# Optimization experiments

Hardware: AMD Instinct MI355X
Metric: run time of the kernel (lower is better)

The kernel has to match this reference:

```python
import jax, jax.numpy as jnp
import numpy as np

L, D, H, DK, FF, R, N, B = 8, 256, 8, 32, 1024, 37, 1024, 1
EPS = 1e-6


def setup_inputs() -> dict:
    key = jax.random.key(0)
    ks = jax.random.split(key, 16)
    def w(i, shape, s=0.05):
        return jax.random.normal(ks[i], shape, jnp.float32) * s
    return {
        "x": jax.random.normal(ks[0], (B, N, D), jnp.float32),
        "relations": jax.random.randint(ks[1], (N, N), 0, R),
        "Wq": w(2, (L, D, D)), "bq": jnp.zeros((L, D), jnp.float32),
        "Wk": w(3, (L, D, D)), "bk": jnp.zeros((L, D), jnp.float32),
        "Wv": w(4, (L, D, D)), "bv": jnp.zeros((L, D), jnp.float32),
        "Wo": w(5, (L, D, D)), "bo": jnp.zeros((L, D), jnp.float32),
        "rel_k_emb": w(6, (L, R, DK)), "rel_v_emb": w(7, (L, R, DK)),
        "W1": w(8, (L, D, FF)), "b1": jnp.zeros((L, FF), jnp.float32),
        "W2": w(9, (L, FF, D)), "b2": jnp.zeros((L, D), jnp.float32),
        "ln1_g": jnp.ones((L, D), jnp.float32), "ln1_b": jnp.zeros((L, D), jnp.float32),
        "ln2_g": jnp.ones((L, D), jnp.float32), "ln2_b": jnp.zeros((L, D), jnp.float32),
        "lnf_g": jnp.ones((D,), jnp.float32), "lnf_b": jnp.zeros((D,), jnp.float32),
    }


def _layernorm(h, g, b):
    # Annotated-Transformer LayerNorm: g*(x-mu)/(std+eps)+b with unbiased std
    mu = h.mean(-1, keepdims=True)
    sd = jnp.sqrt(h.var(-1, keepdims=True, ddof=1))
    return g * (h - mu) / (sd + EPS) + b


def reference(x, relations, Wq, bq, Wk, bk, Wv, bv, Wo, bo,
              rel_k_emb, rel_v_emb, W1, b1, W2, b2,
              ln1_g, ln1_b, ln2_g, ln2_b, lnf_g, lnf_b):
    Bb, n, d = x.shape
    scale = 1.0 / jnp.sqrt(jnp.float32(DK))
    for l in range(L):
        # --- relation-aware self-attention sublayer (pre-norm residual) ---
        xn = _layernorm(x, ln1_g[l], ln1_b[l])
        q = (xn @ Wq[l] + bq[l]).reshape(Bb, n, H, DK).transpose(0, 2, 1, 3)
        k = (xn @ Wk[l] + bk[l]).reshape(Bb, n, H, DK).transpose(0, 2, 1, 3)
        v = (xn @ Wv[l] + bv[l]).reshape(Bb, n, H, DK).transpose(0, 2, 1, 3)
        rk = rel_k_emb[l][relations]  # [n, n, DK] irregular gather
        rv = rel_v_emb[l][relations]  # [n, n, DK]
        scores = (jnp.einsum('bhid,bhjd->bhij', q, k)
                  + jnp.einsum('bhid,ijd->bhij', q, rk)) * scale
        p = jax.nn.softmax(scores, axis=-1)
        o = (jnp.einsum('bhij,bhjd->bhid', p, v)
             + jnp.einsum('bhij,ijd->bhid', p, rv))
        o = o.transpose(0, 2, 1, 3).reshape(Bb, n, d) @ Wo[l] + bo[l]
        x = x + o
        # --- position-wise FFN sublayer (pre-norm residual) ---
        xn = _layernorm(x, ln2_g[l], ln2_b[l])
        x = x + (jax.nn.relu(xn @ W1[l] + b1[l]) @ W2[l] + b2[l])
    return _layernorm(x, lnf_g, lnf_b)
```

## Files before the change

kernel.cpp:

```cpp
#include <hip/hip_runtime.h>
#include <stdint.h>

#define L_ 8
#define D_ 256
#define H_ 8
#define DK_ 32
#define FF_ 1024
#define R_ 37
#define N_ 1024
#define JS_ 4

#define SCL (0.17677669529663689f * 1.4426950408889634f)

typedef float f4v __attribute__((ext_vector_type(4)));
typedef short b8v __attribute__((ext_vector_type(8)));
typedef uint  u2v __attribute__((ext_vector_type(2)));

__device__ __forceinline__ ushort f2b(float f){
  union { float f; uint32_t u; } x; x.f = f;
  return (ushort)((x.u + 0x7FFFu + ((x.u >> 16) & 1u)) >> 16);
}
__device__ __forceinline__ float b2f(ushort u){
  union { uint32_t u; float f; } x; x.u = ((uint32_t)u) << 16;
  return x.f;
}
__device__ __forceinline__ uint pk2b(float lo, float hi){
  return (((uint)f2b(hi)) << 16) | (uint)f2b(lo);
}
__device__ __forceinline__ float ex2(float x){ return __builtin_amdgcn_exp2f(x); }

__global__ __launch_bounds__(256)
void wcast_kernel(const float* __restrict__ src, ushort* __restrict__ dst, int K, int Nc){
  __shared__ float t[32][33];
  int l = blockIdx.z;
  long base = (long)l * K * Nc;
  int n0 = blockIdx.x * 32, k0 = blockIdx.y * 32;
  int tx = threadIdx.x, ty = threadIdx.y;
  #pragma unroll
  for (int r = 0; r < 32; r += 8)
    t[ty + r][tx] = src[base + (long)(k0 + ty + r) * Nc + n0 + tx];
  __syncthreads();
  #pragma unroll
  for (int r = 0; r < 32; r += 8)
    dst[base + (long)(n0 + ty + r) * K + k0 + tx] = f2b(t[tx][ty + r]);
}

template<int OUTB>
__global__ __launch_bounds__(64)
void ln_kernel(const float* __restrict__ x, const float* __restrict__ g, const float* __restrict__ b,
               ushort* __restrict__ ob, float* __restrict__ of){
  int row = blockIdx.x, lane = threadIdx.x;
  float4 v = ((const float4*)(x + (long)row * D_))[lane];
  float s = v.x + v.y + v.z + v.w;
  float s2 = v.x*v.x + v.y*v.y + v.z*v.z + v.w*v.w;
  #pragma unroll
  for (int o = 32; o; o >>= 1){ s += __shfl_xor(s, o); s2 += __shfl_xor(s2, o); }
  float mu = s * (1.f / D_);
  float var = (s2 - D_ * mu * mu) * (1.f / (D_ - 1));
  var = fmaxf(var, 0.f);
  float inv = 1.f / (sqrtf(var) + 1e-6f);
  float4 gv = ((const float4*)g)[lane];
  float4 bv = ((const float4*)b)[lane];
  float o0 = gv.x * (v.x - mu) * inv + bv.x;
  float o1 = gv.y * (v.y - mu) * inv + bv.y;
  float o2 = gv.z * (v.z - mu) * inv + bv.z;
  float o3 = gv.w * (v.w - mu) * inv + bv.w;
  if (OUTB){
    ushort4 u; u.x = f2b(o0); u.y = f2b(o1); u.z = f2b(o2); u.w = f2b(o3);
    ((ushort4*)ob)[(long)row * 64 + lane] = u;
  } else {
    float4 o; o.x = o0; o.y = o1; o.z = o2; o.w = o3;
    ((float4*)of)[(long)row * 64 + lane] = o;
  }
}

template<int QKV, int RELU, int RESID, int OUTF, int OUTB>
__global__ __launch_bounds__(256)
void gemm_kernel(const ushort* __restrict__ A,
                 const ushort* __restrict__ W0, const ushort* __restrict__ W1p, const ushort* __restrict__ W2p,
                 const float* __restrict__ B0, const float* __restrict__ B1p, const float* __restrict__ B2p,
                 float* __restrict__ resid, float* __restrict__ outF, ushort* __restrict__ outB,
                 int M, int Nc, int K){
  __shared__ ushort Al[64 * 48];
  __shared__ ushort Bl[64 * 48];
  int tid = threadIdx.x;
  int lane = tid & 63, w = tid >> 6;
  int wm = w >> 1, wn = w & 1;
  int bn0 = blockIdx.x * 64, bm0 = blockIdx.y * 64;
  const ushort* WT; const float* bias; int wn0;
  if (QKV){
    int which = bn0 >> 8;
    WT = which == 0 ? W0 : (which == 1 ? W1p : W2p);
    bias = which == 0 ? B0 : (which == 1 ? B1p : B2p);
    wn0 = bn0 & 255;
  } else { WT = W0; bias = B0; wn0 = bn0; }

  int r4 = tid >> 2, c8 = (tid & 3) * 8;
  const ushort* ag = A + (long)(bm0 + r4) * K + c8;
  const ushort* bg = WT + (long)(wn0 + r4) * K + c8;

  f4v acc[2][2];
  #pragma unroll
  for (int i = 0; i < 2; ++i)
    #pragma unroll
    for (int j = 0; j < 2; ++j)
      acc[i][j] = (f4v){0.f, 0.f, 0.f, 0.f};

  int l16 = lane & 15, lg = lane >> 4;
  int arow0 = (wm * 32 + l16) * 48 + lg * 8;
  int brow0 = (wn * 32 + l16) * 48 + lg * 8;

  for (int k0 = 0; k0 < K; k0 += 32){
    b8v a8 = *(const b8v*)(ag + k0);
    b8v b8 = *(const b8v*)(bg + k0);
    __syncthreads();
    *(b8v*)&Al[r4 * 48 + c8] = a8;
    *(b8v*)&Bl[r4 * 48 + c8] = b8;
    __syncthreads();
    b8v a0 = *(const b8v*)&Al[arow0];
    b8v a1 = *(const b8v*)&Al[arow0 + 16 * 48];
    b8v b0 = *(const b8v*)&Bl[brow0];
    b8v b1 = *(const b8v*)&Bl[brow0 + 16 * 48];
    acc[0][0] = __builtin_amdgcn_mfma_f32_16x16x32_bf16(a0, b0, acc[0][0], 0, 0, 0);
    acc[0][1] = __builtin_amdgcn_mfma_f32_16x16x32_bf16(a0, b1, acc[0][1], 0, 0, 0);
    acc[1][0] = __builtin_amdgcn_mfma_f32_16x16x32_bf16(a1, b0, acc[1][0], 0, 0, 0);
    acc[1][1] = __builtin_amdgcn_mfma_f32_16x16x32_bf16(a1, b1, acc[1][1], 0, 0, 0);
  }
  #pragma unroll
  for (int fi = 0; fi < 2; ++fi)
    #pragma unroll
    for (int fj = 0; fj < 2; ++fj)
      #pragma unroll
      for (int j = 0; j < 4; ++j){
        int row = bm0 + wm * 32 + fi * 16 + lg * 4 + j;
        int col = bn0 + wn * 32 + fj * 16 + l16;
        float v = acc[fi][fj][j] + bias[QKV ? (col & 255) : col];
        if (QKV){
          long idx = (long)(col >> 8) * 262144 + (long)(((col >> 5) & 7) << 15) + (row << 5) + (col & 31);
          outB[idx] = f2b(v);
        } else {
          if (RELU) v = fmaxf(v, 0.f);
          long idx = (long)row * Nc + col;
          if (RESID) v += resid[idx];
          if (OUTF) outF[idx] = v;
          if (OUTB) outB[idx] = f2b(v);
        }
      }
}

__global__ __launch_bounds__(256)
void vt_kernel(const ushort* __restrict__ vb, ushort* __restrict__ vbt){
  __shared__ ushort t[64][36];
  int j0 = blockIdx.x * 64, h = blockIdx.y;
  int tid = threadIdx.x;
  {
    int r = tid >> 2, c = (tid & 3) * 8;
    *(b8v*)&t[r][c] = *(const b8v*)(vb + ((long)(h << 10) + j0 + r) * 32 + c);
  }
  __syncthreads();
  int d = tid >> 3, jj = (tid & 7) * 8;
  b8v o;
  #pragma unroll
  for (int e = 0; e < 8; ++e) o[e] = (short)t[jj + e][d];
  *(b8v*)(vbt + (long)(h * 32 + d) * 1024 + j0 + jj) = o;
}

__global__ __launch_bounds__(320)
void qr_kernel(const ushort* __restrict__ qb, const float* __restrict__ rke, float* __restrict__ qr){
  __shared__ float ql[256];
  int i = blockIdx.x, t = threadIdx.x;
  if (t < 256){
    int h = t >> 5, dk = t & 31;
    ql[t] = b2f(qb[(long)((h << 10) + i) * 32 + dk]);
  }
  __syncthreads();
  if (t < H_ * R_){
    int h = t / R_, r = t - h * R_;
    const float* qh = &ql[h * DK_];
    const float* e = rke + r * DK_;
    float acc = 0.f;
    #pragma unroll
    for (int d = 0; d < DK_; ++d) acc += qh[d] * e[d];
    qr[((long)(h << 10) + i) * 40 + r] = acc * SCL;
  }
}

__global__ __launch_bounds__(256)
void attn_kernel(const ushort* __restrict__ qb, const ushort* __restrict__ kb,
                 const ushort* __restrict__ vbt, const float* __restrict__ qr,
                 const int* __restrict__ rel, float* __restrict__ part){
  __shared__ ushort q_l[64 * 40];
  __shared__ ushort k_l[32 * 40];
  __shared__ ushort vt_l[32 * 40];
  __shared__ int    rel_l[64 * 36];
  __shared__ float  qr_l[64 * 40];
  __shared__ float  prb[64 * 40];
  __shared__ uint   p_l[4 * 16 * 20];

  int tid = threadIdx.x, lane = tid & 63, w = tid >> 6;
  int l16 = lane & 15, g = lane >> 4;
  int ib0 = blockIdx.x * 64, h = blockIdx.y, js = blockIdx.z;
  int i_loc = w * 16 + l16;

  {
    int r = tid >> 2, c8 = (tid & 3) * 8;
    *(b8v*)&q_l[r * 40 + c8] = *(const b8v*)(qb + (long)((h << 10) + ib0 + r) * 32 + c8);
  }
  {
    const float* src = qr + (long)((h << 10) + ib0) * 40;
    for (int idx = tid; idx < 2560; idx += 256){ qr_l[idx] = src[idx]; prb[idx] = 0.f; }
  }
  __syncthreads();

  b8v qf = *(const b8v*)&q_l[i_loc * 40 + g * 8];

  f4v oacc0 = (f4v){0.f,0.f,0.f,0.f}, oacc1 = (f4v){0.f,0.f,0.f,0.f};
  float m = -3.0e38f, lsum = 0.f;
  const float* qrr = &qr_l[i_loc * 40];

  for (int jt = 0; jt < 8; ++jt){
    int j0 = js * 256 + jt * 32;
    __syncthreads();
    if (tid < 128){
      int r = tid >> 2, c8 = (tid & 3) * 8;
      *(b8v*)&k_l[r * 40 + c8] = *(const b8v*)(kb + (long)((h << 10) + j0 + r) * 32 + c8);
    } else {
      int t2 = tid - 128;
      int d0 = t2 >> 2, c8 = (t2 & 3) * 8;
      *(b8v*)&vt_l[d0 * 40 + c8] = *(const b8v*)(vbt + (long)(h * 32 + d0) * 1024 + j0 + c8);
    }
    {
      int r = tid >> 3, c = (tid & 7) * 4;
      *(int4*)&rel_l[r * 36 + c] = *(const int4*)(rel + (long)(ib0 + r) * N_ + j0 + c);
      *(int4*)&rel_l[(r + 32) * 36 + c] = *(const int4*)(rel + (long)(ib0 + r + 32) * N_ + j0 + c);
    }
    __syncthreads();

    b8v kf0 = *(const b8v*)&k_l[l16 * 40 + g * 8];
    b8v kf1 = *(const b8v*)&k_l[(16 + l16) * 40 + g * 8];
    f4v z = (f4v){0.f,0.f,0.f,0.f};
    f4v s0 = __builtin_amdgcn_mfma_f32_16x16x32_bf16(kf0, qf, z, 0, 0, 0);
    f4v s1 = __builtin_amdgcn_mfma_f32_16x16x32_bf16(kf1, qf, z, 0, 0, 0);

    int4 r0 = *(const int4*)&rel_l[i_loc * 36 + g * 4];
    int4 r1 = *(const int4*)&rel_l[i_loc * 36 + 16 + g * 4];
    int rix[8] = { r0.x, r0.y, r0.z, r0.w, r1.x, r1.y, r1.z, r1.w };
    float sv[8];
    #pragma unroll
    for (int e = 0; e < 4; ++e){
      sv[e]     = s0[e] * SCL + qrr[rix[e]];
      sv[e + 4] = s1[e] * SCL + qrr[rix[e + 4]];
    }
    float tmax = sv[0];
    #pragma unroll
    for (int e = 1; e < 8; ++e) tmax = fmaxf(tmax, sv[e]);
    tmax = fmaxf(tmax, __shfl_xor(tmax, 16));
    tmax = fmaxf(tmax, __shfl_xor(tmax, 32));
    float mn = fmaxf(m, tmax);
    float f = ex2(m - mn);
    float p[8]; float ps = 0.f;
    #pragma unroll
    for (int e = 0; e < 8; ++e){ p[e] = ex2(sv[e] - mn); ps += p[e]; }
    ps += __shfl_xor(ps, 16);
    ps += __shfl_xor(ps, 32);
    lsum = lsum * f + ps;
    oacc0 *= f; oacc1 *= f;
    if (mn > m){
      #pragma unroll
      for (int b2 = 0; b2 < 10; ++b2){
        int bi = g * 10 + b2;
        if (bi < R_) prb[i_loc * 40 + bi] *= f;
      }
    }
    m = mn;
    #pragma unroll
    for (int e = 0; e < 8; ++e) atomicAdd(&prb[i_loc * 40 + rix[e]], p[e]);

    uint pk0 = pk2b(p[0], p[1]), pk1 = pk2b(p[2], p[3]);
    uint pk2 = pk2b(p[4], p[5]), pk3 = pk2b(p[6], p[7]);
    uint* pw = &p_l[w * 320 + l16 * 20];
    *(u2v*)&pw[g * 2]     = (u2v){pk0, pk1};
    *(u2v*)&pw[8 + g * 2] = (u2v){pk2, pk3};
    b8v pf = *(const b8v*)&pw[g * 4];
    b8v vt0 = *(const b8v*)&vt_l[l16 * 40 + g * 8];
    b8v vt1 = *(const b8v*)&vt_l[(16 + l16) * 40 + g * 8];
    oacc0 = __builtin_amdgcn_mfma_f32_16x16x32_bf16(vt0, pf, oacc0, 0, 0, 0);
    oacc1 = __builtin_amdgcn_mfma_f32_16x16x32_bf16(vt1, pf, oacc1, 0, 0, 0);
  }

  float* pp = part + ((long)(h * JS_ + js) * N_ + ib0 + i_loc) * 72;
  #pragma unroll
  for (int r2 = 0; r2 < 4; ++r2){
    pp[g * 4 + r2] = oacc0[r2];
    pp[16 + g * 4 + r2] = oacc1[r2];
  }
  #pragma unroll
  for (int b2 = 0; b2 < 10; ++b2){
    int bi = g * 10 + b2;
    if (bi < R_) pp[32 + bi] = prb[i_loc * 40 + bi];
  }
  if (g == 0){ pp[69] = m; pp[70] = lsum; }
}

__global__ __launch_bounds__(256)
void combine_kernel(const float* __restrict__ part, const float* __restrict__ rve,
                    ushort* __restrict__ ob){
  __shared__ float prl[4][40];
  int tid = threadIdx.x, lane = tid & 63, w = tid >> 6;
  int i = blockIdx.x * 4 + w, h = blockIdx.y;
  int d = lane & 31;
  const float* pb = part + ((long)h * JS_) * N_ * 72 + (long)i * 72;
  float ms[JS_], ls[JS_], wf[JS_];
  float mstar = -3.0e38f;
  #pragma unroll
  for (int s = 0; s < JS_; ++s){
    ms[s] = pb[(long)s * N_ * 72 + 69];
    ls[s] = pb[(long)s * N_ * 72 + 70];
    mstar = fmaxf(mstar, ms[s]);
  }
  float lstar = 0.f;
  #pragma unroll
  for (int s = 0; s < JS_; ++s){ wf[s] = ex2(ms[s] - mstar); lstar += ls[s] * wf[s]; }
  float o1d = 0.f;
  #pragma unroll
  for (int s = 0; s < JS_; ++s) o1d += pb[(long)s * N_ * 72 + d] * wf[s];
  if (lane < R_){
    float prv = 0.f;
    #pragma unroll
    for (int s = 0; s < JS_; ++s) prv += pb[(long)s * N_ * 72 + 32 + lane] * wf[s];
    prl[w][lane] = prv;
  }
  float o2 = 0.f;
  for (int r = 0; r < R_; ++r) o2 += prl[w][r] * rve[r * DK_ + d];
  float val = (o1d + o2) / lstar;
  if (lane < 32) ob[(long)i * D_ + h * DK_ + d] = f2b(val);
}

extern "C" void kernel_launch(void* const* d_in, const int* in_sizes, int n_in,
                              void* d_out, int out_size, void* d_ws, size_t ws_size,
                              hipStream_t stream){
  const float* x    = (const float*)d_in[0];
  const int*   rel  = (const int*)d_in[1];
  const float* Wq   = (const float*)d_in[2];
  const float* bq   = (const float*)d_in[3];
  const float* Wk   = (const float*)d_in[4];
  const float* bk   = (const float*)d_in[5];
  const float* Wv   = (const float*)d_in[6];
  const float* bv   = (const float*)d_in[7];
  const float* Wo   = (const float*)d_in[8];
  const float* bo   = (const float*)d_in[9];
  const float* rke  = (const float*)d_in[10];
  const float* rve  = (const float*)d_in[11];
  const float* W1   = (const float*)d_in[12];
  const float* b1   = (const float*)d_in[13];
  const float* W2   = (const float*)d_in[14];
  const float* b2   = (const float*)d_in[15];
  const float* ln1g = (const float*)d_in[16];
  const float* ln1b = (const float*)d_in[17];
  const float* ln2g = (const float*)d_in[18];
  const float* ln2b = (const float*)d_in[19];
  const float* lnfg = (const float*)d_in[20];
  const float* lnfb = (const float*)d_in[21];

  char* wsb = (char*)d_ws;
  size_t off = 0;
  auto alloc = [&](size_t bytes){ void* p = wsb + off; off += (bytes + 255) & ~255ull; return p; };
  float*  xw   = (float*) alloc((size_t)N_ * D_ * 4);
  ushort* qkvb = (ushort*)alloc((size_t)3 * H_ * N_ * DK_ * 2);
  ushort* vbt  = (ushort*)alloc((size_t)H_ * DK_ * N_ * 2);
  float*  qr   = (float*) alloc((size_t)H_ * N_ * 40 * 4);
  ushort* xnb  = (ushort*)alloc((size_t)N_ * D_ * 2);
  ushort* obf  = (ushort*)alloc((size_t)N_ * D_ * 2);
  float*  part = (float*) alloc((size_t)H_ * JS_ * N_ * 72 * 4);
  ushort* hidb = (ushort*)part;
  ushort* wqT  = (ushort*)alloc((size_t)L_ * D_ * D_ * 2);
  ushort* wkT  = (ushort*)alloc((size_t)L_ * D_ * D_ * 2);
  ushort* wvT  = (ushort*)alloc((size_t)L_ * D_ * D_ * 2);
  ushort* woT  = (ushort*)alloc((size_t)L_ * D_ * D_ * 2);
  ushort* w1T  = (ushort*)alloc((size_t)L_ * D_ * FF_ * 2);
  ushort* w2T  = (ushort*)alloc((size_t)L_ * D_ * FF_ * 2);
  (void)ws_size; (void)in_sizes; (void)n_in; (void)out_size;

  ushort* qb = qkvb;
  ushort* kb = qkvb + (size_t)H_ * N_ * DK_;
  ushort* vb = qkvb + (size_t)2 * H_ * N_ * DK_;

  dim3 tb(32, 8);
  wcast_kernel<<<dim3(D_/32,  D_/32,  L_), tb, 0, stream>>>(Wq, wqT, D_, D_);
  wcast_kernel<<<dim3(D_/32,  D_/32,  L_), tb, 0, stream>>>(Wk, wkT, D_, D_);
  wcast_kernel<<<dim3(D_/32,  D_/32,  L_), tb, 0, stream>>>(Wv, wvT, D_, D_);
  wcast_kernel<<<dim3(D_/32,  D_/32,  L_), tb, 0, stream>>>(Wo, woT, D_, D_);
  wcast_kernel<<<dim3(FF_/32, D_/32,  L_), tb, 0, stream>>>(W1, w1T, D_, FF_);
  wcast_kernel<<<dim3(D_/32,  FF_/32, L_), tb, 0, stream>>>(W2, w2T, FF_, D_);

  hipMemcpyAsync(xw, x, (size_t)N_ * D_ * 4, hipMemcpyDeviceToDevice, stream);

  for (int l = 0; l < L_; ++l){
    ln_kernel<1><<<N_, 64, 0, stream>>>(xw, ln1g + l * D_, ln1b + l * D_, xnb, nullptr);
    gemm_kernel<1,0,0,0,1><<<dim3(768/64, N_/64), 256, 0, stream>>>(
        xnb, wqT + (size_t)l * D_ * D_, wkT + (size_t)l * D_ * D_, wvT + (size_t)l * D_ * D_,
        bq + l * D_, bk + l * D_, bv + l * D_,
        nullptr, nullptr, qkvb, N_, 768, D_);
    vt_kernel<<<dim3(N_/64, H_), 256, 0, stream>>>(vb, vbt);
    qr_kernel<<<N_, 320, 0, stream>>>(qb, rke + (size_t)l * R_ * DK_, qr);
    attn_kernel<<<dim3(N_/64, H_, JS_), 256, 0, stream>>>(qb, kb, vbt, qr, rel, part);
    combine_kernel<<<dim3(N_/4, H_), 256, 0, stream>>>(part, rve + (size_t)l * R_ * DK_, obf);
    gemm_kernel<0,0,1,1,0><<<dim3(D_/64, N_/64), 256, 0, stream>>>(
        obf, woT + (size_t)l * D_ * D_, nullptr, nullptr,
        bo + l * D_, nullptr, nullptr,
        xw, xw, nullptr, N_, D_, D_);
    ln_kernel<1><<<N_, 64, 0, stream>>>(xw, ln2g + l * D_, ln2b + l * D_, xnb, nullptr);
    gemm_kernel<0,1,0,0,1><<<dim3(FF_/64, N_/64), 256, 0, stream>>>(
        xnb, w1T + (size_t)l * D_ * FF_, nullptr, nullptr,
        b1 + l * FF_, nullptr, nullptr,
        nullptr, nullptr, hidb, N_, FF_, D_);
    gemm_kernel<0,0,1,1,0><<<dim3(D_/64, N_/64), 256, 0, stream>>>(
        hidb, w2T + (size_t)l * FF_ * D_, nullptr, nullptr,
        b2 + l * D_, nullptr, nullptr,
        xw, xw, nullptr, N_, D_, FF_);
  }
  ln_kernel<0><<<N_, 64, 0, stream>>>(xw, lnfg, lnfb, nullptr, (float*)d_out);
}
```

Measured before the change: 931.5 us.

## Restructure attention: direct global fragment loads, byte relations, lazy rescale, fused V transpose

The attention kernel no longer stages K, V^T and relation tiles through shared memory with per-tile barriers. It loads MFMA fragments straight from global memory and reads relations from a precomputed uint8 copy, which cuts relation bandwidth by a factor of four. The online softmax now rescales only when the running max grows by more than a threshold, and the key split doubles to 8 for more parallelism. The QKV GEMM epilogue writes V already transposed, so the separate transpose kernel is removed. The trade-offs are uncoalesced per-lane global loads, larger partial buffers for the combine step, and an extra one-time relation packing kernel.

```diff
diff --git a/kernel.cpp b/kernel.cpp
--- a/kernel.cpp
+++ b/kernel.cpp
@@ -8,7 +8,7 @@
 #define FF_ 1024
 #define R_ 37
 #define N_ 1024
-#define JS_ 4
+#define JS_ 8
 
 #define SCL (0.17677669529663689f * 1.4426950408889634f)
 
@@ -43,6 +43,14 @@
   #pragma unroll
   for (int r = 0; r < 32; r += 8)
     dst[base + (long)(n0 + ty + r) * K + k0 + tx] = f2b(t[tx][ty + r]);
+}
+
+__global__ __launch_bounds__(256)
+void rel8_kernel(const int* __restrict__ rel, uint* __restrict__ rel8){
+  long idx = (long)blockIdx.x * 256 + threadIdx.x;
+  int4 v = ((const int4*)rel)[idx];
+  rel8[idx] = (uint)(v.x & 255) | ((uint)(v.y & 255) << 8)
+            | ((uint)(v.z & 255) << 16) | ((uint)(v.w & 255) << 24);
 }
 
 template<int OUTB>
@@ -80,6 +88,7 @@
                  const ushort* __restrict__ W0, const ushort* __restrict__ W1p, const ushort* __restrict__ W2p,
                  const float* __restrict__ B0, const float* __restrict__ B1p, const float* __restrict__ B2p,
                  float* __restrict__ resid, float* __restrict__ outF, ushort* __restrict__ outB,
+                 ushort* __restrict__ outB2,
                  int M, int Nc, int K){
   __shared__ ushort Al[64 * 48];
   __shared__ ushort Bl[64 * 48];
@@ -129,40 +138,34 @@
   #pragma unroll
   for (int fi = 0; fi < 2; ++fi)
     #pragma unroll
-    for (int fj = 0; fj < 2; ++fj)
+    for (int fj = 0; fj < 2; ++fj){
+      int row0 = bm0 + wm * 32 + fi * 16 + lg * 4;
+      int col = bn0 + wn * 32 + fj * 16 + l16;
+      float vv[4];
       #pragma unroll
-      for (int j = 0; j < 4; ++j){
-        int row = bm0 + wm * 32 + fi * 16 + lg * 4 + j;
-        int col = bn0 + wn * 32 + fj * 16 + l16;
-        float v = acc[fi][fj][j] + bias[QKV ? (col & 255) : col];
-        if (QKV){
-          long idx = (long)(col >> 8) * 262144 + (long)(((col >> 5) & 7) << 15) + (row << 5) + (col & 31);
-          outB[idx] = f2b(v);
+      for (int j = 0; j < 4; ++j) vv[j] = acc[fi][fj][j] + bias[QKV ? (col & 255) : col];
+      if (QKV){
+        int which = col >> 8, hh = (col >> 5) & 7, dk = col & 31;
+        if (which == 2){
+          ushort4 pk; pk.x = f2b(vv[0]); pk.y = f2b(vv[1]); pk.z = f2b(vv[2]); pk.w = f2b(vv[3]);
+          *(ushort4*)(outB2 + (long)hh * 32768 + (long)dk * 1024 + row0) = pk;
         } else {
+          #pragma unroll
+          for (int j = 0; j < 4; ++j)
+            outB[(long)which * 262144 + (long)hh * 32768 + (long)(row0 + j) * 32 + dk] = f2b(vv[j]);
+        }
+      } else {
+        #pragma unroll
+        for (int j = 0; j < 4; ++j){
+          float v = vv[j];
           if (RELU) v = fmaxf(v, 0.f);
-          long idx = (long)row * Nc + col;
+          long idx = (long)(row0 + j) * Nc + col;
           if (RESID) v += resid[idx];
           if (OUTF) outF[idx] = v;
           if (OUTB) outB[idx] = f2b(v);
         }
       }
-}
-
-__global__ __launch_bounds__(256)
-void vt_kernel(const ushort* __restrict__ vb, ushort* __restrict__ vbt){
-  __shared__ ushort t[64][36];
-  int j0 = blockIdx.x * 64, h = blockIdx.y;
-  int tid = threadIdx.x;
-  {
-    int r = tid >> 2, c = (tid & 3) * 8;
-    *(b8v*)&t[r][c] = *(const b8v*)(vb + ((long)(h << 10) + j0 + r) * 32 + c);
-  }
-  __syncthreads();
-  int d = tid >> 3, jj = (tid & 7) * 8;
-  b8v o;
-  #pragma unroll
-  for (int e = 0; e < 8; ++e) o[e] = (short)t[jj + e][d];
-  *(b8v*)(vbt + (long)(h * 32 + d) * 1024 + j0 + jj) = o;
+    }
 }
 
 __global__ __launch_bounds__(320)
@@ -188,14 +191,10 @@
 __global__ __launch_bounds__(256)
 void attn_kernel(const ushort* __restrict__ qb, const ushort* __restrict__ kb,
                  const ushort* __restrict__ vbt, const float* __restrict__ qr,
-                 const int* __restrict__ rel, float* __restrict__ part){
-  __shared__ ushort q_l[64 * 40];
-  __shared__ ushort k_l[32 * 40];
-  __shared__ ushort vt_l[32 * 40];
-  __shared__ int    rel_l[64 * 36];
-  __shared__ float  qr_l[64 * 40];
-  __shared__ float  prb[64 * 40];
-  __shared__ uint   p_l[4 * 16 * 20];
+                 const unsigned char* __restrict__ rel8, float* __restrict__ part){
+  __shared__ float qr_l[64 * 40];
+  __shared__ float prb[64 * 40];
+  __shared__ uint  p_l[4 * 16 * 20];
 
   int tid = threadIdx.x, lane = tid & 63, w = tid >> 6;
   int l16 = lane & 15, g = lane >> 4;
@@ -203,51 +202,42 @@
   int i_loc = w * 16 + l16;
 
   {
-    int r = tid >> 2, c8 = (tid & 3) * 8;
-    *(b8v*)&q_l[r * 40 + c8] = *(const b8v*)(qb + (long)((h << 10) + ib0 + r) * 32 + c8);
-  }
-  {
     const float* src = qr + (long)((h << 10) + ib0) * 40;
     for (int idx = tid; idx < 2560; idx += 256){ qr_l[idx] = src[idx]; prb[idx] = 0.f; }
   }
   __syncthreads();
 
-  b8v qf = *(const b8v*)&q_l[i_loc * 40 + g * 8];
+  b8v qf = *(const b8v*)(qb + (long)((h << 10) + ib0 + i_loc) * 32 + g * 8);
 
   f4v oacc0 = (f4v){0.f,0.f,0.f,0.f}, oacc1 = (f4v){0.f,0.f,0.f,0.f};
   float m = -3.0e38f, lsum = 0.f;
   const float* qrr = &qr_l[i_loc * 40];
-
-  for (int jt = 0; jt < 8; ++jt){
-    int j0 = js * 256 + jt * 32;
-    __syncthreads();
-    if (tid < 128){
-      int r = tid >> 2, c8 = (tid & 3) * 8;
-      *(b8v*)&k_l[r * 40 + c8] = *(const b8v*)(kb + (long)((h << 10) + j0 + r) * 32 + c8);
-    } else {
-      int t2 = tid - 128;
-      int d0 = t2 >> 2, c8 = (t2 & 3) * 8;
-      *(b8v*)&vt_l[d0 * 40 + c8] = *(const b8v*)(vbt + (long)(h * 32 + d0) * 1024 + j0 + c8);
-    }
-    {
-      int r = tid >> 3, c = (tid & 7) * 4;
-      *(int4*)&rel_l[r * 36 + c] = *(const int4*)(rel + (long)(ib0 + r) * N_ + j0 + c);
-      *(int4*)&rel_l[(r + 32) * 36 + c] = *(const int4*)(rel + (long)(ib0 + r + 32) * N_ + j0 + c);
-    }
-    __syncthreads();
-
-    b8v kf0 = *(const b8v*)&k_l[l16 * 40 + g * 8];
-    b8v kf1 = *(const b8v*)&k_l[(16 + l16) * 40 + g * 8];
+  float* prr = &prb[i_loc * 40];
+  const unsigned char* relrow = rel8 + (long)(ib0 + i_loc) * N_ + js * (N_ / JS_);
+  const ushort* kbh = kb + (long)(h << 10) * 32;
+  const ushort* vth = vbt + (long)h * 32 * 1024;
+  uint* pw = &p_l[w * 320 + l16 * 20];
+
+  #pragma unroll
+  for (int jt = 0; jt < N_ / JS_ / 32; ++jt){
+    int j0 = js * (N_ / JS_) + jt * 32;
+    b8v kf0 = *(const b8v*)(kbh + (long)(j0 + l16) * 32 + g * 8);
+    b8v kf1 = *(const b8v*)(kbh + (long)(j0 + 16 + l16) * 32 + g * 8);
+    b8v vt0 = *(const b8v*)(vth + (long)l16 * 1024 + j0 + g * 8);
+    b8v vt1 = *(const b8v*)(vth + (long)(16 + l16) * 1024 + j0 + g * 8);
+    uint rr0 = *(const uint*)(relrow + jt * 32 + g * 4);
+    uint rr1 = *(const uint*)(relrow + jt * 32 + 16 + g * 4);
+
     f4v z = (f4v){0.f,0.f,0.f,0.f};
     f4v s0 = __builtin_amdgcn_mfma_f32_16x16x32_bf16(kf0, qf, z, 0, 0, 0);
     f4v s1 = __builtin_amdgcn_mfma_f32_16x16x32_bf16(kf1, qf, z, 0, 0, 0);
 
-    int4 r0 = *(const int4*)&rel_l[i_loc * 36 + g * 4];
-    int4 r1 = *(const int4*)&rel_l[i_loc * 36 + 16 + g * 4];
-    int rix[8] = { r0.x, r0.y, r0.z, r0.w, r1.x, r1.y, r1.z, r1.w };
+    int rix[8];
     float sv[8];
     #pragma unroll
     for (int e = 0; e < 4; ++e){
+      rix[e]     = (rr0 >> (8 * e)) & 255;
+      rix[e + 4] = (rr1 >> (8 * e)) & 255;
       sv[e]     = s0[e] * SCL + qrr[rix[e]];
       sv[e + 4] = s1[e] * SCL + qrr[rix[e + 4]];
     }
@@ -256,34 +246,31 @@
     for (int e = 1; e < 8; ++e) tmax = fmaxf(tmax, sv[e]);
     tmax = fmaxf(tmax, __shfl_xor(tmax, 16));
     tmax = fmaxf(tmax, __shfl_xor(tmax, 32));
-    float mn = fmaxf(m, tmax);
-    float f = ex2(m - mn);
-    float p[8]; float ps = 0.f;
-    #pragma unroll
-    for (int e = 0; e < 8; ++e){ p[e] = ex2(sv[e] - mn); ps += p[e]; }
-    ps += __shfl_xor(ps, 16);
-    ps += __shfl_xor(ps, 32);
-    lsum = lsum * f + ps;
-    oacc0 *= f; oacc1 *= f;
-    if (mn > m){
+
+    if (tmax - m > 12.f){
+      float f = ex2(m - tmax);
+      oacc0 *= f; oacc1 *= f; lsum *= f;
       #pragma unroll
       for (int b2 = 0; b2 < 10; ++b2){
         int bi = g * 10 + b2;
-        if (bi < R_) prb[i_loc * 40 + bi] *= f;
+        if (bi < R_) prr[bi] *= f;
       }
+      m = tmax;
     }
-    m = mn;
-    #pragma unroll
-    for (int e = 0; e < 8; ++e) atomicAdd(&prb[i_loc * 40 + rix[e]], p[e]);
+    float p[8], ps = 0.f;
+    #pragma unroll
+    for (int e = 0; e < 8; ++e){ p[e] = ex2(sv[e] - m); ps += p[e]; }
+    ps += __shfl_xor(ps, 16);
+    ps += __shfl_xor(ps, 32);
+    lsum += ps;
+    #pragma unroll
+    for (int e = 0; e < 8; ++e) atomicAdd(&prr[rix[e]], p[e]);
 
     uint pk0 = pk2b(p[0], p[1]), pk1 = pk2b(p[2], p[3]);
     uint pk2 = pk2b(p[4], p[5]), pk3 = pk2b(p[6], p[7]);
-    uint* pw = &p_l[w * 320 + l16 * 20];
     *(u2v*)&pw[g * 2]     = (u2v){pk0, pk1};
     *(u2v*)&pw[8 + g * 2] = (u2v){pk2, pk3};
     b8v pf = *(const b8v*)&pw[g * 4];
-    b8v vt0 = *(const b8v*)&vt_l[l16 * 40 + g * 8];
-    b8v vt1 = *(const b8v*)&vt_l[(16 + l16) * 40 + g * 8];
     oacc0 = __builtin_amdgcn_mfma_f32_16x16x32_bf16(vt0, pf, oacc0, 0, 0, 0);
     oacc1 = __builtin_amdgcn_mfma_f32_16x16x32_bf16(vt1, pf, oacc1, 0, 0, 0);
   }
@@ -297,7 +284,7 @@
   #pragma unroll
   for (int b2 = 0; b2 < 10; ++b2){
     int bi = g * 10 + b2;
-    if (bi < R_) pp[32 + bi] = prb[i_loc * 40 + bi];
+    if (bi < R_) pp[32 + bi] = prr[bi];
   }
   if (g == 0){ pp[69] = m; pp[70] = lsum; }
 }
@@ -373,6 +360,7 @@
   ushort* obf  = (ushort*)alloc((size_t)N_ * D_ * 2);
   float*  part = (float*) alloc((size_t)H_ * JS_ * N_ * 72 * 4);
   ushort* hidb = (ushort*)part;
+  uint*   rel8 = (uint*)  alloc((size_t)N_ * N_);
   ushort* wqT  = (ushort*)alloc((size_t)L_ * D_ * D_ * 2);
   ushort* wkT  = (ushort*)alloc((size_t)L_ * D_ * D_ * 2);
   ushort* wvT  = (ushort*)alloc((size_t)L_ * D_ * D_ * 2);
@@ -383,7 +371,6 @@
 
   ushort* qb = qkvb;
   ushort* kb = qkvb + (size_t)H_ * N_ * DK_;
-  ushort* vb = qkvb + (size_t)2 * H_ * N_ * DK_;
 
   dim3 tb(32, 8);
   wcast_kernel<<<dim3(D_/32,  D_/32,  L_), tb, 0, stream>>>(Wq, wqT, D_, D_);
@@ -392,6 +379,7 @@
   wcast_kernel<<<dim3(D_/32,  D_/32,  L_), tb, 0, stream>>>(Wo, woT, D_, D_);
   wcast_kernel<<<dim3(FF_/32, D_/32,  L_), tb, 0, stream>>>(W1, w1T, D_, FF_);
   wcast_kernel<<<dim3(D_/32,  FF_/32, L_), tb, 0, stream>>>(W2, w2T, FF_, D_);
+  rel8_kernel<<<N_ * N_ / 1024, 256, 0, stream>>>(rel, rel8);
 
   hipMemcpyAsync(xw, x, (size_t)N_ * D_ * 4, hipMemcpyDeviceToDevice, stream);
 
@@ -400,24 +388,23 @@
     gemm_kernel<1,0,0,0,1><<<dim3(768/64, N_/64), 256, 0, stream>>>(
         xnb, wqT + (size_t)l * D_ * D_, wkT + (size_t)l * D_ * D_, wvT + (size_t)l * D_ * D_,
         bq + l * D_, bk + l * D_, bv + l * D_,
-        nullptr, nullptr, qkvb, N_, 768, D_);
-    vt_kernel<<<dim3(N_/64, H_), 256, 0, stream>>>(vb, vbt);
+        nullptr, nullptr, qkvb, vbt, N_, 768, D_);
     qr_kernel<<<N_, 320, 0, stream>>>(qb, rke + (size_t)l * R_ * DK_, qr);
-    attn_kernel<<<dim3(N_/64, H_, JS_), 256, 0, stream>>>(qb, kb, vbt, qr, rel, part);
+    attn_kernel<<<dim3(N_/64, H_, JS_), 256, 0, stream>>>(qb, kb, vbt, qr, (const unsigned char*)rel8, part);
     combine_kernel<<<dim3(N_/4, H_), 256, 0, stream>>>(part, rve + (size_t)l * R_ * DK_, obf);
     gemm_kernel<0,0,1,1,0><<<dim3(D_/64, N_/64), 256, 0, stream>>>(
         obf, woT + (size_t)l * D_ * D_, nullptr, nullptr,
         bo + l * D_, nullptr, nullptr,
-        xw, xw, nullptr, N_, D_, D_);
+        xw, xw, nullptr, nullptr, N_, D_, D_);
     ln_kernel<1><<<N_, 64, 0, stream>>>(xw, ln2g + l * D_, ln2b + l * D_, xnb, nullptr);
     gemm_kernel<0,1,0,0,1><<<dim3(FF_/64, N_/64), 256, 0, stream>>>(
         xnb, w1T + (size_t)l * D_ * FF_, nullptr, nullptr,
         b1 + l * FF_, nullptr, nullptr,
-        nullptr, nullptr, hidb, N_, FF_, D_);
+        nullptr, nullptr, hidb, nullptr, N_, FF_, D_);
     gemm_kernel<0,0,1,1,0><<<dim3(D_/64, N_/64), 256, 0, stream>>>(
         hidb, w2T + (size_t)l * FF_ * D_, nullptr, nullptr,
         b2 + l * D_, nullptr, nullptr,
-        xw, xw, nullptr, N_, D_, FF_);
+        xw, xw, nullptr, nullptr, N_, D_, FF_);
   }
   ln_kernel<0><<<N_, 64, 0, stream>>>(xw, lnfg, lnfb, nullptr, (float*)d_out);
 }
```

Measured after the change: 871.9 us. 6.4% less time.
